# Optimization experiments

Measured on AMD Instinct MI355X. Metric: run time of the kernel, lower is better.

## Reference

```python
import jax, jax.numpy as jnp
import numpy as np

N_HEAD = 16
N_KV_HEAD = 4
N_EMBD = 2048
HEAD_DIM = N_EMBD // N_HEAD
RMS_EPS = float(np.finfo(np.float32).eps)  # torch F.rms_norm default eps


def setup_inputs() -> dict:
    key = jax.random.key(0)
    ks = jax.random.split(key, 7)
    B, T = 2, 2048
    s = 0.02
    return {
        "x": jax.random.normal(ks[0], (B, T, N_EMBD), jnp.float32),
        "cos": jax.random.uniform(ks[1], (T, 1, HEAD_DIM), jnp.float32),
        "sin": jax.random.uniform(ks[2], (T, 1, HEAD_DIM), jnp.float32),
        "wq": jax.random.normal(ks[3], (N_HEAD * HEAD_DIM, N_EMBD), jnp.float32) * s,
        "wk": jax.random.normal(ks[4], (N_KV_HEAD * HEAD_DIM, N_EMBD), jnp.float32) * s,
        "wv": jax.random.normal(ks[5], (N_KV_HEAD * HEAD_DIM, N_EMBD), jnp.float32) * s,
        "wproj": jax.random.normal(ks[6], (N_EMBD, N_EMBD), jnp.float32) * s,
    }


def _rotate_half(x):
    h = x.shape[-1] // 2
    return jnp.concatenate([-x[..., h:], x[..., :h]], axis=-1)


def _apply_rope(x, cos, sin):  # x: [B, T, H, D]; cos/sin: [T, 1, D]
    return x * cos + _rotate_half(x) * sin


def _rms_norm(x):
    var = jnp.mean(jnp.square(x), axis=-1, keepdims=True)
    return x * jax.lax.rsqrt(var + RMS_EPS)


def reference(x, cos, sin, wq, wk, wv, wproj):
    B, T, C = x.shape
    group = N_HEAD // N_KV_HEAD
    q = (x @ wq.T).reshape(B, T, N_HEAD, HEAD_DIM)
    k = (x @ wk.T).reshape(B, T, N_KV_HEAD, HEAD_DIM)
    v = (x @ wv.T).reshape(B, T, N_KV_HEAD, HEAD_DIM)
    q = _rms_norm(_apply_rope(q, cos, sin))  # RoPE then QK RMSNorm
    k = _rms_norm(_apply_rope(k, cos, sin))
    # to [B, H, T, D]; expand kv heads for GQA
    q = q.transpose(0, 2, 1, 3)
    k = jnp.repeat(k.transpose(0, 2, 1, 3), group, axis=1)
    v = jnp.repeat(v.transpose(0, 2, 1, 3), group, axis=1)
    scale = 1.0 / jnp.sqrt(jnp.asarray(HEAD_DIM, x.dtype))
    scores = jnp.einsum('bhqd,bhkd->bhqk', q, k) * scale
    causal = jnp.tril(jnp.ones((T, T), bool))
    scores = jnp.where(causal, scores, jnp.asarray(-jnp.inf, scores.dtype))
    attn = jax.nn.softmax(scores, axis=-1)
    y = jnp.einsum('bhqk,bhkd->bhqd', attn, v)
    y = y.transpose(0, 2, 1, 3).reshape(B, T, C)
    return y @ wproj.T
```

## Files before the change

### kernel.cpp

```cpp
#include <hip/hip_runtime.h>
#include <hip/hip_bf16.h>

typedef __hip_bfloat16 bf16;
typedef __attribute__((ext_vector_type(8))) __bf16 bf16x8;
typedef __attribute__((ext_vector_type(4))) float f32x4;

#define MFMA16(a, b, c) __builtin_amdgcn_mfma_f32_16x16x32_bf16((a), (b), (c), 0, 0, 0)

#define BT 4096
#define CE 2048
#define NQKV 3072
#define TSEQ 2048
#define HD 128

#define QSCALE (0.08838834764831845f * 1.4426950408889634f)
#define M2 16.3222f

__device__ __forceinline__ void gld16(const void* g, void* l)
{
    __builtin_amdgcn_global_load_lds(
        (const __attribute__((address_space(1))) void*)g,
        (__attribute__((address_space(3))) void*)l, 16, 0, 0);
}

__global__ void detect_dtype(const unsigned short* __restrict__ x, int* __restrict__ flag)
{
    __shared__ int cnt;
    if (threadIdx.x == 0) cnt = 0;
    __syncthreads();
    unsigned short w = x[2 * threadIdx.x];
    int e = (w >> 7) & 0xFF;
    atomicAdd(&cnt, (e >= 117 && e <= 130) ? 1 : 0);
    __syncthreads();
    if (threadIdx.x == 0) *flag = (cnt < 128) ? 1 : 0;
}

__device__ __forceinline__ void stage8(short* dst, const void* src, size_t eoff, bool f32)
{
    if (f32) {
        const float* s = (const float*)src + eoff;
        float4 f0 = *(const float4*)s;
        float4 f1 = *(const float4*)(s + 4);
        bf16x8 v;
        v[0] = (__bf16)f0.x; v[1] = (__bf16)f0.y; v[2] = (__bf16)f0.z; v[3] = (__bf16)f0.w;
        v[4] = (__bf16)f1.x; v[5] = (__bf16)f1.y; v[6] = (__bf16)f1.z; v[7] = (__bf16)f1.w;
        *(bf16x8*)dst = v;
    } else {
        *(uint4*)dst = *(const uint4*)((const bf16*)src + eoff);
    }
}

__device__ __forceinline__ float ldf(const void* p, int i, bool f32)
{
    return f32 ? ((const float*)p)[i] : __bfloat162float(((const bf16*)p)[i]);
}

__global__ __launch_bounds__(256)
void conv_bf16(const void* __restrict__ src, bf16* __restrict__ dst,
               const int* __restrict__ flagp)
{
    const bool f = *flagp != 0;
    size_t i8 = (size_t)blockIdx.x * 256 + threadIdx.x;
    stage8((short*)(dst + i8 * 8), src, i8 * 8, f);
}

__global__ __launch_bounds__(256)
void gemm_bt(const void* __restrict__ A, const bf16* __restrict__ W,
             void* __restrict__ C, int M, int N, int K, int lda,
             int aGate, int oGate, const int* __restrict__ flagp)
{
    __shared__ short As[128][32];
    __shared__ short Bs[128][32];

    const int f = *flagp;
    const bool aF = aGate && f, oF = oGate && f;

    const int tid   = threadIdx.x;
    const int lane  = tid & 63;
    const int wid   = tid >> 6;
    const int row16 = lane & 15;
    const int quad  = lane >> 4;
    const int wr    = wid >> 1;
    const int wc    = wid & 1;
    const int m0    = blockIdx.y * 128;
    const int n0    = blockIdx.x * 128;

    const int rl4 = wid * 16 + (lane >> 2);
    const int c8  = (lane & 3) * 8;

    f32x4 acc[4][4];
#pragma unroll
    for (int i = 0; i < 4; i++)
#pragma unroll
        for (int j = 0; j < 4; j++)
            acc[i][j] = (f32x4){0.f, 0.f, 0.f, 0.f};

    for (int k0 = 0; k0 < K; k0 += 32) {
#pragma unroll
        for (int i = 0; i < 2; i++) {
            int r = i * 64 + rl4;
            gld16(W + (size_t)(n0 + r) * K + k0 + c8, &Bs[r][c8]);
        }
        if (!aF) {
#pragma unroll
            for (int i = 0; i < 2; i++) {
                int r = i * 64 + rl4;
                gld16((const bf16*)A + (size_t)(m0 + r) * lda + k0 + c8, &As[r][c8]);
            }
        } else {
#pragma unroll
            for (int i = 0; i < 2; i++) {
                int c = i * 256 + tid;
                int row = c >> 2, col = (c & 3) << 3;
                stage8(&As[row][col], A, (size_t)(m0 + row) * lda + k0 + col, true);
            }
        }
        __syncthreads();

        bf16x8 af[4], bfv[4];
#pragma unroll
        for (int mi = 0; mi < 4; mi++)
            af[mi] = *(const bf16x8*)&As[wr * 64 + mi * 16 + row16][quad * 8];
#pragma unroll
        for (int ni = 0; ni < 4; ni++)
            bfv[ni] = *(const bf16x8*)&Bs[wc * 64 + ni * 16 + row16][quad * 8];
#pragma unroll
        for (int mi = 0; mi < 4; mi++)
#pragma unroll
            for (int ni = 0; ni < 4; ni++)
                acc[mi][ni] = MFMA16(af[mi], bfv[ni], acc[mi][ni]);
        __syncthreads();
    }

#pragma unroll
    for (int mi = 0; mi < 4; mi++) {
        int rowb = m0 + wr * 64 + mi * 16 + quad * 4;
#pragma unroll
        for (int ni = 0; ni < 4; ni++) {
            int col = n0 + wc * 64 + ni * 16 + row16;
#pragma unroll
            for (int r = 0; r < 4; r++) {
                size_t idx = (size_t)(rowb + r) * N + col;
                float  v   = acc[mi][ni][r];
                if (oF) ((float*)C)[idx] = v;
                else    ((bf16*)C)[idx]  = __float2bfloat16(v);
            }
        }
    }
}

template<int MI>
__global__ __launch_bounds__(512, 2)
void gemmP(const bf16* __restrict__ A, const bf16* __restrict__ W,
           void* __restrict__ C, int M, int N, int K, int lda,
           int oGate, const int* __restrict__ flagp)
{
    constexpr int BM     = MI * 32;
    constexpr int ABYTES = BM * 128;
    constexpr int AUL    = ABYTES / 8192;

    __shared__ __bf16 As[2][BM][64];
    __shared__ __bf16 Bs[2][256][64];

    const bool oF = oGate && (*flagp != 0);

    const int tid   = threadIdx.x;
    const int lane  = tid & 63;
    const int wid   = tid >> 6;
    const int row16 = lane & 15;
    const int quad  = lane >> 4;
    const int wr    = wid >> 2;
    const int wc    = wid & 3;
    const int m0    = blockIdx.y * BM;
    const int n0    = blockIdx.x * 256;
    const int NT    = K >> 6;

    const int srow = tid >> 3;
    const int sc8  = ((tid & 7) ^ (srow & 7)) * 8;
    const bf16* Ag = A + (size_t)(m0 + srow) * lda + sc8;
    const bf16* Bg = W + (size_t)(n0 + srow) * K   + sc8;
    char* const AsB = (char*)As;
    char* const BsB = (char*)Bs;
    const int sdst = tid * 16;

    auto stA = [&](int kt, int b) {
#pragma unroll
        for (int u = 0; u < AUL; ++u)
            gld16(Ag + (size_t)(u * 64) * lda + kt * 64,
                  AsB + b * ABYTES + u * 8192 + sdst);
    };
    auto stB = [&](int kt, int b) {
#pragma unroll
        for (int u = 0; u < 4; ++u)
            gld16(Bg + (size_t)(u * 64) * K + kt * 64,
                  BsB + b * 32768 + u * 8192 + sdst);
    };

    const int swz  = ((quad ^ (row16 & 7)) * 16);
    const int swz1 = (((4 + quad) ^ (row16 & 7)) * 16);
    const int aRow = wr * (MI * 16) + row16;
    const int bRow = wc * 64 + row16;

    auto ldA = [&](int b, int mi, int kk) -> bf16x8 {
        return *(const bf16x8*)(AsB + b * ABYTES + (aRow + mi * 16) * 128
                                + (kk ? swz1 : swz));
    };
    auto ldB = [&](int b, int ni, int kk) -> bf16x8 {
        return *(const bf16x8*)(BsB + b * 32768 + (bRow + ni * 16) * 128
                                + (kk ? swz1 : swz));
    };

    f32x4 acc[MI][4];
#pragma unroll
    for (int i = 0; i < MI; i++)
#pragma unroll
        for (int j = 0; j < 4; j++)
            acc[i][j] = (f32x4){0.f, 0.f, 0.f, 0.f};

    stA(0, 0); stB(0, 0);
    asm volatile("s_waitcnt vmcnt(0)" ::: "memory");
    __builtin_amdgcn_s_barrier();
    __builtin_amdgcn_sched_barrier(0);

    for (int t = 0; t < NT; ++t) {
        const int rb = t & 1;
        const int wb = rb ^ 1;

        bf16x8 bfr[4][2];
#pragma unroll
        for (int ni = 0; ni < 4; ni++)
#pragma unroll
            for (int kk = 0; kk < 2; kk++)
                bfr[ni][kk] = ldB(rb, ni, kk);
        bf16x8 a0[2][2];
#pragma unroll
        for (int i = 0; i < 2; i++)
#pragma unroll
            for (int kk = 0; kk < 2; kk++)
                a0[i][kk] = ldA(rb, i, kk);

        if (t + 1 < NT) { stB(t + 1, wb); stA(t + 1, wb); }

        __builtin_amdgcn_s_setprio(1);
#pragma unroll
        for (int kk = 0; kk < 2; kk++)
#pragma unroll
            for (int i = 0; i < 2; i++)
#pragma unroll
                for (int ni = 0; ni < 4; ni++)
                    acc[i][ni] = MFMA16(a0[i][kk], bfr[ni][kk], acc[i][ni]);
        __builtin_amdgcn_s_setprio(0);

#pragma unroll
        for (int p = 1; p < MI / 2; ++p) {
            bf16x8 ap[2][2];
#pragma unroll
            for (int i = 0; i < 2; i++)
#pragma unroll
                for (int kk = 0; kk < 2; kk++)
                    ap[i][kk] = ldA(rb, 2 * p + i, kk);
            __builtin_amdgcn_s_setprio(1);
#pragma unroll
            for (int kk = 0; kk < 2; kk++)
#pragma unroll
                for (int i = 0; i < 2; i++)
#pragma unroll
                    for (int ni = 0; ni < 4; ni++)
                        acc[2 * p + i][ni] =
                            MFMA16(ap[i][kk], bfr[ni][kk], acc[2 * p + i][ni]);
            __builtin_amdgcn_s_setprio(0);
        }

        asm volatile("s_waitcnt vmcnt(0)" ::: "memory");
        __builtin_amdgcn_s_barrier();
        __builtin_amdgcn_sched_barrier(0);
    }

#pragma unroll
    for (int mi = 0; mi < MI; mi++) {
        int rowb = m0 + wr * (MI * 16) + mi * 16 + quad * 4;
#pragma unroll
        for (int ni = 0; ni < 4; ni++) {
            int col = n0 + wc * 64 + ni * 16 + row16;
#pragma unroll
            for (int r = 0; r < 4; r++) {
                size_t idx = (size_t)(rowb + r) * N + col;
                float  v   = acc[mi][ni][r];
                if (oF) ((float*)C)[idx] = v;
                else    ((bf16*)C)[idx]  = __float2bfloat16(v);
            }
        }
    }
}

__global__ __launch_bounds__(256)
void rope_rms(bf16* __restrict__ qkv, const void* __restrict__ cosp,
              const void* __restrict__ sinp, const int* __restrict__ flagp)
{
    const bool f = *flagp != 0;
    const int wg   = blockIdx.x * 4 + (threadIdx.x >> 6);
    const int lane = threadIdx.x & 63;
    const int s    = wg % 20;
    const int m    = wg / 20;
    const int t    = m & (TSEQ - 1);

    const int col = (s < 16) ? s * HD : CE + (s - 16) * HD;
    bf16* p = qkv + (size_t)m * NQKV + col;

    float xlo = __bfloat162float(p[lane]);
    float xhi = __bfloat162float(p[lane + 64]);
    float cl  = ldf(cosp, t * HD + lane, f);
    float sl  = ldf(sinp, t * HD + lane, f);
    float ch  = ldf(cosp, t * HD + 64 + lane, f);
    float sh  = ldf(sinp, t * HD + 64 + lane, f);

    float rlo = xlo * cl - xhi * sl;
    float rhi = xhi * ch + xlo * sh;

    float ss = rlo * rlo + rhi * rhi;
#pragma unroll
    for (int off = 32; off > 0; off >>= 1)
        ss += __shfl_xor(ss, off, 64);
    float inv = rsqrtf(ss * (1.0f / 128.0f) + 1.1920929e-07f);
    if (s < 16) inv *= QSCALE;

    p[lane]      = __float2bfloat16(rlo * inv);
    p[lane + 64] = __float2bfloat16(rhi * inv);
}

__global__ __launch_bounds__(256)
void vtrans(const bf16* __restrict__ qkv, bf16* __restrict__ vt)
{
    int idx = blockIdx.x * 256 + threadIdx.x;
    int t  = idx & (TSEQ - 1);
    int d  = (idx >> 11) & 127;
    int bh = idx >> 18;
    vt[idx] = qkv[((size_t)((bh >> 2) * TSEQ + t)) * NQKV + 2560 + (bh & 3) * HD + d];
}

__global__ __launch_bounds__(512, 4)
void attn(bf16* __restrict__ qkv, const bf16* __restrict__ vt)
{
    __shared__ __bf16 Ks[2][64][128];
    __shared__ __bf16 Vs[2][128][64];
    __shared__ __bf16 Pl[8][16][64];

    const int tid   = threadIdx.x;
    const int lane  = tid & 63;
    const int wid   = tid >> 6;
    const int row16 = lane & 15;
    const int quad  = lane >> 4;
    const int b   = blockIdx.y >> 2;
    const int hk  = blockIdx.y & 3;
    const int h   = hk * 4 + (wid & 3);
    const int mh  = wid >> 2;

    const int xi  = 63 - blockIdx.x;
    const int nkt = (xi >> 1) + 1;
    const int qr0 = xi * 32 + mh * 16;

    const bf16* Kp = qkv + ((size_t)(b * TSEQ)) * NQKV + CE + hk * HD;
    const bf16* Vp = vt + ((size_t)(b * 4 + hk) * HD) * TSEQ;

    char* const KsB = (char*)Ks;
    char* const VsB = (char*)Vs;
    char* const PlB = (char*)Pl;

    auto stage = [&](int buf, int k0) {
#pragma unroll
        for (int i = 0; i < 2; i++) {
            int kr = (wid << 3) + i * 4 + (lane >> 4);
            int kc = (lane & 15) ^ (kr & 7);
            gld16(Kp + (size_t)(k0 + kr) * NQKV + kc * 8,
                  KsB + buf * 16384 + ((wid << 3) + i * 4) * 256 + lane * 16);
            int vr = (wid << 4) + i * 8 + (lane >> 3);
            int vc = (lane & 7) ^ (vr & 7);
            gld16(Vp + (size_t)vr * TSEQ + k0 + vc * 8,
                  VsB + buf * 16384 + ((wid << 4) + i * 8) * 128 + lane * 16);
        }
    };

    const bf16* Q = qkv + ((size_t)(b * TSEQ + qr0)) * NQKV + h * HD;
    bf16x8 aq[4];
#pragma unroll
    for (int ds = 0; ds < 4; ds++)
        aq[ds] = *(const bf16x8*)(Q + (size_t)row16 * NQKV + ds * 32 + quad * 8);

    f32x4 o[8];
#pragma unroll
    for (int dt = 0; dt < 8; dt++) o[dt] = (f32x4){0.f, 0.f, 0.f, 0.f};
    float lsum[4] = {0.f, 0.f, 0.f, 0.f};

    stage(0, 0);
    __syncthreads();

    for (int t = 0; t < nkt; ++t) {
        const int cur = t & 1;
        if (t + 1 < nkt) stage(cur ^ 1, (t + 1) * 64);

        f32x4 s[4];
#pragma unroll
        for (int kg = 0; kg < 4; kg++) s[kg] = (f32x4){0.f, 0.f, 0.f, 0.f};
        __builtin_amdgcn_s_setprio(1);
#pragma unroll
        for (int ds = 0; ds < 4; ds++) {
#pragma unroll
            for (int kg = 0; kg < 4; kg++) {
                int krow = kg * 16 + row16;
                int phys = (ds * 4 + quad) ^ (row16 & 7);
                bf16x8 kf = *(const bf16x8*)(KsB + cur * 16384 + krow * 256 + phys * 16);
                s[kg] = MFMA16(aq[ds], kf, s[kg]);
            }
        }
        __builtin_amdgcn_s_setprio(0);

        const bool diag = (t == nkt - 1);
        const int  k0   = t * 64;
        const int  r16h = row16 >> 3;
        const int  r16l = (row16 & 7) * 2;
#pragma unroll
        for (int r = 0; r < 4; r++) {
            float pv[4];
            int prow = quad * 4 + r;
            int qrow = qr0 + prow;
#pragma unroll
            for (int kg = 0; kg < 4; kg++) {
                float e = __builtin_amdgcn_exp2f(s[kg][r] - M2);
                pv[kg] = (!diag || (k0 + kg * 16 + row16 <= qrow)) ? e : 0.f;
            }
            lsum[r] += (pv[0] + pv[1]) + (pv[2] + pv[3]);
#pragma unroll
            for (int kg = 0; kg < 4; kg++)
                *(__bf16*)(PlB + wid * 2048 + prow * 128
                           + (((kg * 2 + r16h) ^ (prow & 7)) << 4) + r16l)
                    = (__bf16)pv[kg];
        }
        __asm__ volatile("" ::: "memory");

        __builtin_amdgcn_s_setprio(1);
#pragma unroll
        for (int c = 0; c < 2; c++) {
            bf16x8 pf = *(const bf16x8*)(PlB + wid * 2048 + row16 * 128
                                         + ((((c << 2) + quad) ^ (row16 & 7)) << 4));
#pragma unroll
            for (int dt = 0; dt < 8; dt++) {
                int vrow = dt * 16 + row16;
                int phys = (c * 4 + quad) ^ (row16 & 7);
                bf16x8 vf = *(const bf16x8*)(VsB + cur * 16384 + vrow * 128 + phys * 16);
                o[dt] = MFMA16(pf, vf, o[dt]);
            }
        }
        __builtin_amdgcn_s_setprio(0);
        __asm__ volatile("" ::: "memory");
        __syncthreads();
    }

#pragma unroll
    for (int r = 0; r < 4; r++) {
        float l = lsum[r];
#pragma unroll
        for (int off = 1; off < 16; off <<= 1)
            l += __shfl_xor(l, off, 64);
        float rl = 1.0f / l;
        int trow = qr0 + quad * 4 + r;
        bf16* dst = qkv + ((size_t)(b * TSEQ + trow)) * NQKV + h * HD;
#pragma unroll
        for (int dt = 0; dt < 8; dt++)
            dst[dt * 16 + row16] = __float2bfloat16(o[dt][r] * rl);
    }
}

extern "C" void kernel_launch(void* const* d_in, const int* in_sizes, int n_in,
                              void* d_out, int out_size, void* d_ws, size_t ws_size,
                              hipStream_t stream)
{
    bf16* qkv   = (bf16*)d_ws;
    bf16* vt    = qkv + (size_t)BT * NQKV;
    bf16* wqkvb = vt + (size_t)2 * 4 * HD * TSEQ;
    int* flagp  = (int*)(wqkvb + (size_t)NQKV * CE);
    bf16* xb    = wqkvb + (size_t)NQKV * CE + 16;

    const size_t need = ((size_t)BT * NQKV + (size_t)2 * 4 * HD * TSEQ
                         + (size_t)NQKV * CE + 16 + (size_t)BT * CE) * sizeof(bf16);
    const bool useXb = ws_size >= need;

    detect_dtype<<<1, 256, 0, stream>>>((const unsigned short*)d_in[0], flagp);

    conv_bf16<<<(2048 * 2048 / 8) / 256, 256, 0, stream>>>(d_in[3], wqkvb, flagp);
    conv_bf16<<<(512 * 2048 / 8) / 256, 256, 0, stream>>>(d_in[4], wqkvb + (size_t)2048 * 2048, flagp);
    conv_bf16<<<(512 * 2048 / 8) / 256, 256, 0, stream>>>(d_in[5], wqkvb + (size_t)2560 * 2048, flagp);

    if (useXb) {
        conv_bf16<<<(BT * CE / 8) / 256, 256, 0, stream>>>(d_in[0], xb, flagp);
        gemmP<8><<<dim3(NQKV / 256, BT / 256), 512, 0, stream>>>(
            xb, wqkvb, qkv, BT, NQKV, CE, CE, 0, flagp);
    } else {
        gemm_bt<<<dim3(NQKV / 128, BT / 128), 256, 0, stream>>>(
            d_in[0], wqkvb, qkv, BT, NQKV, CE, CE, 1, 0, flagp);
    }

    conv_bf16<<<(2048 * 2048 / 8) / 256, 256, 0, stream>>>(d_in[6], wqkvb, flagp);

    vtrans<<<(2 * 4 * HD * TSEQ) / 256, 256, 0, stream>>>(qkv, vt);

    rope_rms<<<(BT * 20) / 4, 256, 0, stream>>>(qkv, d_in[1], d_in[2], flagp);

    attn<<<dim3(64, 2 * 4), 512, 0, stream>>>(qkv, vt);

    if (useXb) {
        gemmP<4><<<dim3(CE / 256, BT / 128), 512, 0, stream>>>(
            qkv, wqkvb, d_out, BT, CE, CE, NQKV, 1, flagp);
    } else {
        gemm_bt<<<dim3(CE / 128, BT / 128), 256, 0, stream>>>(
            qkv, wqkvb, d_out, BT, CE, CE, NQKV, 0, 1, flagp);
    }
}
```

Measured before the change: 345.7 us.

## Balance causal attention work, tile V transpose via LDS, swizzle GEMM block order

The attention kernel now pairs query block p with block 63-p in one workgroup, so each block does a near-constant amount of causal work, and the grid is halved. The occupancy hint drops to 2 blocks per CU. The V transpose moves from a scalar gather to an LDS-tiled transpose with 16-byte loads and stores. The GEMM remaps block IDs with an 8-way swizzle meant to improve cache locality across XCDs. The trade-off is fewer attention blocks in flight, which may reduce latency hiding.

```diff
diff --git a/kernel.cpp b/kernel.cpp
--- a/kernel.cpp
+++ b/kernel.cpp
@@ -164,6 +164,13 @@
 
     const bool oF = oGate && (*flagp != 0);
 
+    const int gx  = gridDim.x;
+    const int lin = blockIdx.y * gx + blockIdx.x;
+    const int cpx = (gx * gridDim.y) >> 3;
+    const int swzid = (lin & 7) * cpx + (lin >> 3);
+    const int bx = swzid % gx;
+    const int by = swzid / gx;
+
     const int tid   = threadIdx.x;
     const int lane  = tid & 63;
     const int wid   = tid >> 6;
@@ -171,8 +178,8 @@
     const int quad  = lane >> 4;
     const int wr    = wid >> 2;
     const int wc    = wid & 3;
-    const int m0    = blockIdx.y * BM;
-    const int n0    = blockIdx.x * 256;
+    const int m0    = by * BM;
+    const int n0    = bx * 256;
     const int NT    = K >> 6;
 
     const int srow = tid >> 3;
@@ -331,14 +338,39 @@
 __global__ __launch_bounds__(256)
 void vtrans(const bf16* __restrict__ qkv, bf16* __restrict__ vt)
 {
-    int idx = blockIdx.x * 256 + threadIdx.x;
-    int t  = idx & (TSEQ - 1);
-    int d  = (idx >> 11) & 127;
-    int bh = idx >> 18;
-    vt[idx] = qkv[((size_t)((bh >> 2) * TSEQ + t)) * NQKV + 2560 + (bh & 3) * HD + d];
-}
-
-__global__ __launch_bounds__(512, 4)
+    __shared__ __bf16 tl[64][136];
+
+    const int tid = threadIdx.x;
+    const int bh  = blockIdx.x >> 5;
+    const int t0  = (blockIdx.x & 31) * 64;
+    const int b   = bh >> 2;
+    const int hk  = bh & 3;
+
+    const bf16* src = qkv + ((size_t)(b * TSEQ + t0)) * NQKV + 2560 + hk * HD;
+#pragma unroll
+    for (int it = 0; it < 4; ++it) {
+        int idx  = it * 256 + tid;
+        int trow = idx >> 4;
+        int dcol = (idx & 15) * 8;
+        *(uint4*)&tl[trow][dcol] = *(const uint4*)(src + (size_t)trow * NQKV + dcol);
+    }
+    __syncthreads();
+
+    bf16* dst = vt + ((size_t)(bh * HD)) * TSEQ + t0;
+#pragma unroll
+    for (int it = 0; it < 4; ++it) {
+        int idx  = it * 256 + tid;
+        int drow = idx >> 3;
+        int tcol = (idx & 7) * 8;
+        bf16x8 v;
+#pragma unroll
+        for (int j = 0; j < 8; ++j)
+            v[j] = tl[tcol + j][drow];
+        *(bf16x8*)(dst + (size_t)drow * TSEQ + tcol) = v;
+    }
+}
+
+__global__ __launch_bounds__(512, 2)
 void attn(bf16* __restrict__ qkv, const bf16* __restrict__ vt)
 {
     __shared__ __bf16 Ks[2][64][128];
@@ -354,10 +386,7 @@
     const int hk  = blockIdx.y & 3;
     const int h   = hk * 4 + (wid & 3);
     const int mh  = wid >> 2;
-
-    const int xi  = 63 - blockIdx.x;
-    const int nkt = (xi >> 1) + 1;
-    const int qr0 = xi * 32 + mh * 16;
+    const int p   = blockIdx.x;
 
     const bf16* Kp = qkv + ((size_t)(b * TSEQ)) * NQKV + CE + hk * HD;
     const bf16* Vp = vt + ((size_t)(b * 4 + hk) * HD) * TSEQ;
@@ -380,93 +409,100 @@
         }
     };
 
-    const bf16* Q = qkv + ((size_t)(b * TSEQ + qr0)) * NQKV + h * HD;
-    bf16x8 aq[4];
-#pragma unroll
-    for (int ds = 0; ds < 4; ds++)
-        aq[ds] = *(const bf16x8*)(Q + (size_t)row16 * NQKV + ds * 32 + quad * 8);
-
-    f32x4 o[8];
-#pragma unroll
-    for (int dt = 0; dt < 8; dt++) o[dt] = (f32x4){0.f, 0.f, 0.f, 0.f};
-    float lsum[4] = {0.f, 0.f, 0.f, 0.f};
-
-    stage(0, 0);
-    __syncthreads();
-
-    for (int t = 0; t < nkt; ++t) {
-        const int cur = t & 1;
-        if (t + 1 < nkt) stage(cur ^ 1, (t + 1) * 64);
-
-        f32x4 s[4];
-#pragma unroll
-        for (int kg = 0; kg < 4; kg++) s[kg] = (f32x4){0.f, 0.f, 0.f, 0.f};
-        __builtin_amdgcn_s_setprio(1);
-#pragma unroll
-        for (int ds = 0; ds < 4; ds++) {
-#pragma unroll
-            for (int kg = 0; kg < 4; kg++) {
-                int krow = kg * 16 + row16;
-                int phys = (ds * 4 + quad) ^ (row16 & 7);
-                bf16x8 kf = *(const bf16x8*)(KsB + cur * 16384 + krow * 256 + phys * 16);
-                s[kg] = MFMA16(aq[ds], kf, s[kg]);
-            }
-        }
-        __builtin_amdgcn_s_setprio(0);
-
-        const bool diag = (t == nkt - 1);
-        const int  k0   = t * 64;
-        const int  r16h = row16 >> 3;
-        const int  r16l = (row16 & 7) * 2;
+    for (int pass = 0; pass < 2; ++pass) {
+        const int xi  = pass ? 63 - p : p;
+        const int nkt = (xi >> 1) + 1;
+        const int qr0 = xi * 32 + mh * 16;
+
+        const bf16* Q = qkv + ((size_t)(b * TSEQ + qr0)) * NQKV + h * HD;
+        bf16x8 aq[4];
+#pragma unroll
+        for (int ds = 0; ds < 4; ds++)
+            aq[ds] = *(const bf16x8*)(Q + (size_t)row16 * NQKV + ds * 32 + quad * 8);
+
+        f32x4 o[8];
+#pragma unroll
+        for (int dt = 0; dt < 8; dt++) o[dt] = (f32x4){0.f, 0.f, 0.f, 0.f};
+        float lsum[4] = {0.f, 0.f, 0.f, 0.f};
+
+        __syncthreads();
+        stage(0, 0);
+        __syncthreads();
+
+        for (int t = 0; t < nkt; ++t) {
+            const int cur = t & 1;
+            if (t + 1 < nkt) stage(cur ^ 1, (t + 1) * 64);
+
+            f32x4 s[4];
+#pragma unroll
+            for (int kg = 0; kg < 4; kg++) s[kg] = (f32x4){0.f, 0.f, 0.f, 0.f};
+            __builtin_amdgcn_s_setprio(1);
+#pragma unroll
+            for (int ds = 0; ds < 4; ds++) {
+#pragma unroll
+                for (int kg = 0; kg < 4; kg++) {
+                    int krow = kg * 16 + row16;
+                    int phys = (ds * 4 + quad) ^ (row16 & 7);
+                    bf16x8 kf = *(const bf16x8*)(KsB + cur * 16384 + krow * 256 + phys * 16);
+                    s[kg] = MFMA16(aq[ds], kf, s[kg]);
+                }
+            }
+            __builtin_amdgcn_s_setprio(0);
+
+            const bool diag = (t == nkt - 1);
+            const int  k0   = t * 64;
+            const int  r16h = row16 >> 3;
+            const int  r16l = (row16 & 7) * 2;
+#pragma unroll
+            for (int r = 0; r < 4; r++) {
+                float pv[4];
+                int prow = quad * 4 + r;
+                int qrow = qr0 + prow;
+#pragma unroll
+                for (int kg = 0; kg < 4; kg++) {
+                    float e = __builtin_amdgcn_exp2f(s[kg][r] - M2);
+                    pv[kg] = (!diag || (k0 + kg * 16 + row16 <= qrow)) ? e : 0.f;
+                }
+                lsum[r] += (pv[0] + pv[1]) + (pv[2] + pv[3]);
+#pragma unroll
+                for (int kg = 0; kg < 4; kg++)
+                    *(__bf16*)(PlB + wid * 2048 + prow * 128
+                               + (((kg * 2 + r16h) ^ (prow & 7)) << 4) + r16l)
+                        = (__bf16)pv[kg];
+            }
+            __asm__ volatile("" ::: "memory");
+
+            __builtin_amdgcn_s_setprio(1);
+#pragma unroll
+            for (int c = 0; c < 2; c++) {
+                bf16x8 pf = *(const bf16x8*)(PlB + wid * 2048 + row16 * 128
+                                             + ((((c << 2) + quad) ^ (row16 & 7)) << 4));
+#pragma unroll
+                for (int dt = 0; dt < 8; dt++) {
+                    int vrow = dt * 16 + row16;
+                    int phys = (c * 4 + quad) ^ (row16 & 7);
+                    bf16x8 vf = *(const bf16x8*)(VsB + cur * 16384 + vrow * 128 + phys * 16);
+                    o[dt] = MFMA16(pf, vf, o[dt]);
+                }
+            }
+            __builtin_amdgcn_s_setprio(0);
+            __asm__ volatile("" ::: "memory");
+            __syncthreads();
+        }
+
 #pragma unroll
         for (int r = 0; r < 4; r++) {
-            float pv[4];
-            int prow = quad * 4 + r;
-            int qrow = qr0 + prow;
-#pragma unroll
-            for (int kg = 0; kg < 4; kg++) {
-                float e = __builtin_amdgcn_exp2f(s[kg][r] - M2);
-                pv[kg] = (!diag || (k0 + kg * 16 + row16 <= qrow)) ? e : 0.f;
-            }
-            lsum[r] += (pv[0] + pv[1]) + (pv[2] + pv[3]);
-#pragma unroll
-            for (int kg = 0; kg < 4; kg++)
-                *(__bf16*)(PlB + wid * 2048 + prow * 128
-                           + (((kg * 2 + r16h) ^ (prow & 7)) << 4) + r16l)
-                    = (__bf16)pv[kg];
-        }
-        __asm__ volatile("" ::: "memory");
-
-        __builtin_amdgcn_s_setprio(1);
-#pragma unroll
-        for (int c = 0; c < 2; c++) {
-            bf16x8 pf = *(const bf16x8*)(PlB + wid * 2048 + row16 * 128
-                                         + ((((c << 2) + quad) ^ (row16 & 7)) << 4));
-#pragma unroll
-            for (int dt = 0; dt < 8; dt++) {
-                int vrow = dt * 16 + row16;
-                int phys = (c * 4 + quad) ^ (row16 & 7);
-                bf16x8 vf = *(const bf16x8*)(VsB + cur * 16384 + vrow * 128 + phys * 16);
-                o[dt] = MFMA16(pf, vf, o[dt]);
-            }
-        }
-        __builtin_amdgcn_s_setprio(0);
-        __asm__ volatile("" ::: "memory");
-        __syncthreads();
-    }
-
-#pragma unroll
-    for (int r = 0; r < 4; r++) {
-        float l = lsum[r];
-#pragma unroll
-        for (int off = 1; off < 16; off <<= 1)
-            l += __shfl_xor(l, off, 64);
-        float rl = 1.0f / l;
-        int trow = qr0 + quad * 4 + r;
-        bf16* dst = qkv + ((size_t)(b * TSEQ + trow)) * NQKV + h * HD;
-#pragma unroll
-        for (int dt = 0; dt < 8; dt++)
-            dst[dt * 16 + row16] = __float2bfloat16(o[dt][r] * rl);
+            float l = lsum[r];
+#pragma unroll
+            for (int off = 1; off < 16; off <<= 1)
+                l += __shfl_xor(l, off, 64);
+            float rl = 1.0f / l;
+            int trow = qr0 + quad * 4 + r;
+            bf16* dst = qkv + ((size_t)(b * TSEQ + trow)) * NQKV + h * HD;
+#pragma unroll
+            for (int dt = 0; dt < 8; dt++)
+                dst[dt * 16 + row16] = __float2bfloat16(o[dt][r] * rl);
+        }
     }
 }
 
@@ -501,11 +537,11 @@
 
     conv_bf16<<<(2048 * 2048 / 8) / 256, 256, 0, stream>>>(d_in[6], wqkvb, flagp);
 
-    vtrans<<<(2 * 4 * HD * TSEQ) / 256, 256, 0, stream>>>(qkv, vt);
+    vtrans<<<256, 256, 0, stream>>>(qkv, vt);
 
     rope_rms<<<(BT * 20) / 4, 256, 0, stream>>>(qkv, d_in[1], d_in[2], flagp);
 
-    attn<<<dim3(64, 2 * 4), 512, 0, stream>>>(qkv, vt);
+    attn<<<dim3(32, 2 * 4), 512, 0, stream>>>(qkv, vt);
 
     if (useXb) {
         gemmP<4><<<dim3(CE / 256, BT / 128), 512, 0, stream>>>(
```

New measurement: 321.0 us. 1.08x faster.
